# Performance work log

Hardware: AMD Instinct MI355X
Metric: run time of the kernel (lower is better)

## Reference

```python
import jax, jax.numpy as jnp
import numpy as np


def swish(x):
    return x * jax.nn.sigmoid(x)


def setup_inputs() -> dict:
    key = jax.random.key(0)
    ks = jax.random.split(key, 12)
    b, n, c, h, dg, hid = 4, 512, 256, 8, 6, 16

    def lin(k, i, o):
        return jax.random.normal(k, (i, o), jnp.float32) / np.float32(np.sqrt(i))

    return {
        "pairwise_g": jax.random.normal(ks[0], (b, n, n, dg), jnp.float32),
        "coset_functions": jax.random.normal(ks[1], (b, n, c), jnp.float32),
        "fc_q_w": lin(ks[2], c, c), "fc_q_b": jnp.zeros((c,), jnp.float32),
        "fc_k_w": lin(ks[3], c, c), "fc_k_b": jnp.zeros((c,), jnp.float32),
        "in_w": lin(ks[4], c, c), "in_b": jnp.zeros((c,), jnp.float32),
        "out_w": lin(ks[5], c, c), "out_b": jnp.zeros((c,), jnp.float32),
        "loc_w1": jax.random.normal(ks[6], (h, dg, hid), jnp.float32) / np.float32(np.sqrt(dg)),
        "loc_b1": jnp.zeros((h, hid), jnp.float32),
        "loc_w2": jax.random.normal(ks[7], (h, hid, hid), jnp.float32) / np.float32(np.sqrt(hid)),
        "loc_b2": jnp.zeros((h, hid), jnp.float32),
        "loc_w3": jax.random.normal(ks[8], (h, hid, 1), jnp.float32) / np.float32(np.sqrt(hid)),
        "loc_b3": jnp.zeros((h, 1), jnp.float32),
        "mask": jax.random.randint(ks[9], (4, 512), 0, 2) > 0,
    }


def reference(pairwise_g, coset_functions, fc_q_w, fc_q_b, fc_k_w, fc_k_b,
              in_w, in_b, out_w, out_b,
              loc_w1, loc_b1, loc_w2, loc_b2, loc_w3, loc_b3, mask):
    # nbhd_idx = arange(n) in the original (dense neighborhoods), so all
    # advanced-index gathers are identities and are expressed as broadcasts.
    b, n, c = coset_functions.shape
    h = loc_w1.shape[0]
    d = c // h

    # DotProductKernel: scores scaled by sqrt(embed_dim) = sqrt(c)
    Q = (coset_functions @ fc_q_w + fc_q_b).reshape(b, n, h, d)
    K = (coset_functions @ fc_k_w + fc_k_b).reshape(b, n, h, d)
    A_feat = jnp.einsum('bnhd,bmhd->bnmh', Q, K) / np.float32(np.sqrt(c))  # (b,n,m,h)

    # MultiheadWeightNet location kernel: per-head 3-layer MLP with swish
    # after every linear (LieConv-style LinearBNact blocks), out_dim=1.
    x = swish(jnp.einsum('bnmg,hgk->bnmhk', pairwise_g, loc_w1) + loc_b1)
    x = swish(jnp.einsum('bnmhk,hkj->bnmhj', x, loc_w2) + loc_b2)
    A_loc = swish(jnp.einsum('bnmhk,hko->bnmho', x, loc_w3) + loc_b3)[..., 0]  # (b,n,m,h)

    pre = A_loc + A_feat
    nbhd_mask = mask[:, None, :, None]          # mask over keys j: (b,1,m,1)
    pre = jnp.where(nbhd_mask, pre, jnp.float32(-1e38))
    att = jax.nn.softmax(pre, axis=2)           # softmax over neighbor dim m

    V = (coset_functions @ in_w + in_b).reshape(b, n, h, d)  # input_linear
    out = jnp.einsum('bnmh,bmhd->bnhd', att, V).reshape(b, n, c)
    return out @ out_w + out_b                  # output_linear; (b,n,c_out)
```

## Files before the change

### kernel.cpp

```cpp
#include <hip/hip_runtime.h>
#include <math.h>

namespace {

constexpr int kB = 4, kN = 512, kC = 256, kH = 8, kDG = 6, kHID = 16;

constexpr int S_QH = 20;
constexpr int S_W1 = 68;
constexpr int S_W2 = 132;
constexpr int S_B  = 17;
constexpr int S_AT = 516;

typedef _Float16 half2v __attribute__((ext_vector_type(2)));

__device__ __forceinline__ float swishf(float x) {
    return x * __builtin_amdgcn_rcpf(1.0f + __expf(-x));
}

__device__ __forceinline__ unsigned pk16(float a, float b) {
    unsigned short ha = __builtin_bit_cast(unsigned short, (_Float16)a);
    unsigned short hb = __builtin_bit_cast(unsigned short, (_Float16)b);
    return (unsigned)ha | ((unsigned)hb << 16);
}

__device__ __forceinline__ unsigned pkrtz(float a, float b) {
#if __has_builtin(__builtin_amdgcn_cvt_pkrtz)
    return __builtin_bit_cast(unsigned, __builtin_amdgcn_cvt_pkrtz(a, b));
#else
    return pk16(a, b);
#endif
}

__device__ __forceinline__ float fdot2u(unsigned a, unsigned b, float c) {
#if __has_builtin(__builtin_amdgcn_fdot2)
    return __builtin_amdgcn_fdot2(__builtin_bit_cast(half2v, a),
                                  __builtin_bit_cast(half2v, b), c, false);
#else
    half2v ha = __builtin_bit_cast(half2v, a);
    half2v hb = __builtin_bit_cast(half2v, b);
    return c + (float)ha[0] * (float)hb[0] + (float)ha[1] * (float)hb[1];
#endif
}

__global__ __launch_bounds__(256) void k_qkvc(
    const float* __restrict__ x,
    const float* __restrict__ wq, const float* __restrict__ bq,
    const float* __restrict__ wk, const float* __restrict__ bk,
    const float* __restrict__ wv, const float* __restrict__ bv,
    unsigned* __restrict__ Qh, unsigned* __restrict__ Kh,
    float* __restrict__ V,
    const unsigned char* __restrict__ mraw,
    int* __restrict__ list, int* __restrict__ meta) {
    const int t = threadIdx.x;

    if (blockIdx.x == 512) {
        __shared__ int s_isbool;
        if (t == 0) s_isbool = 0;
        __syncthreads();
        int found = 0;
        for (int i = t; i < kB * kN; i += 256)
            if ((i & 3) && mraw[i]) found = 1;
        if (found) atomicOr(&s_isbool, 1);
        __syncthreads();
        const int isb = s_isbool;
        const int b = t >> 6, lane = t & 63;
        const int* mi = (const int*)mraw;
        int base = 0;
        for (int c = 0; c < 8; ++c) {
            const int m = c * 64 + lane;
            const int idx = b * kN + m;
            const int valid = isb ? (mraw[idx] != 0) : (mi[idx] != 0);
            unsigned long long bal = __ballot(valid);
            int rank = (int)__popcll(bal & ((1ull << lane) - 1ull));
            if (valid) list[b * kN + base + rank] = m;
            base += (int)__popcll(bal);
        }
        for (int i = base + lane; i < kN; i += 64)
            list[b * kN + i] = (base == 0) ? i : 0;
        if (lane == 0) {
            meta[b] = (base == 0) ? kN : base;
            meta[4 + b] = (base == 0);
        }
        return;
    }

    __shared__ float sx[4][kC];
    const int r0 = blockIdx.x * 4;
    #pragma unroll
    for (int r = 0; r < 4; ++r) sx[r][t] = x[(r0 + r) * kC + t];
    __syncthreads();
    float aq[4] = {}, ak[4] = {}, av[4] = {};
    for (int k = 0; k < kC; ++k) {
        const float q = wq[k * kC + t];
        const float kk = wk[k * kC + t];
        const float v = wv[k * kC + t];
        #pragma unroll
        for (int r = 0; r < 4; ++r) {
            aq[r] += sx[r][k] * q;
            ak[r] += sx[r][k] * kk;
            av[r] += sx[r][k] * v;
        }
    }
    const float qb = bq[t], kb = bk[t], vb = bv[t];
    #pragma unroll
    for (int r = 0; r < 4; ++r) {
        const float qv = aq[r] + qb;
        const float kv = ak[r] + kb;
        V[(r0 + r) * kC + t] = av[r] + vb;
        const float qn = __shfl_down(qv, 1);
        const float kn = __shfl_down(kv, 1);
        if ((t & 1) == 0) {
            Qh[(r0 + r) * (kC / 2) + (t >> 1)] = pk16(qv, qn);
            Kh[(r0 + r) * (kC / 2) + (t >> 1)] = pk16(kv, kn);
        }
    }
}

__global__ __launch_bounds__(256, 4) void k_attn(
    const float* __restrict__ G,
    const unsigned* __restrict__ Qh,
    const unsigned* __restrict__ Kh,
    const float* __restrict__ V,
    const float* __restrict__ w1, const float* __restrict__ b1,
    const float* __restrict__ w2, const float* __restrict__ b2,
    const float* __restrict__ w3, const float* __restrict__ b3,
    const int* __restrict__ list, const int* __restrict__ meta,
    float* __restrict__ out) {
    __shared__ __align__(16) unsigned sQh[kH * S_QH];
    __shared__ __align__(16) uint4 sG4[kN];
    __shared__ int sList[kN];
    __shared__ __align__(16) unsigned sW1[kH * S_W1];
    __shared__ __align__(16) unsigned sW2[kH * S_W2];
    __shared__ float sB1[kH * S_B];
    __shared__ float sB2[kH * S_B];
    __shared__ float sW3[kH * S_B];
    __shared__ float sB3[kH];
    __shared__ float sAtt[kH * S_AT];
    __shared__ float sInv[kH];

    const int bn = blockIdx.x;
    const int b = bn >> 9;
    const int t = threadIdx.x;

    if (t < kH * S_QH) {
        const int h = t / S_QH, r = t % S_QH;
        sQh[t] = (r < 16) ? Qh[bn * (kC / 2) + h * 16 + r] : 0u;
    }
    sList[t] = list[b * kN + t];
    sList[t + 256] = list[b * kN + t + 256];
    #pragma unroll 1
    for (int rep = 0; rep < 2; ++rep) {
        const int m = t + rep * 256;
        const float* gp = G + ((size_t)bn * kN + m) * kDG;
        uint4 gw;
        gw.x = pkrtz(gp[0], gp[1]);
        gw.y = pkrtz(gp[2], gp[3]);
        gw.z = pkrtz(gp[4], gp[5]);
        gw.w = 0;
        sG4[m] = gw;
    }
    if (t < 128) {
        const int h = t >> 4, k = t & 15;
        const float* wp = w1 + (h * kDG) * kHID + k;
        sW1[h * S_W1 + k * 4 + 0] = pk16(wp[0], wp[16]);
        sW1[h * S_W1 + k * 4 + 1] = pk16(wp[32], wp[48]);
        sW1[h * S_W1 + k * 4 + 2] = pk16(wp[64], wp[80]);
        sW1[h * S_W1 + k * 4 + 3] = 0;
        sB1[h * S_B + k] = b1[h * kHID + k];
        sB2[h * S_B + k] = b2[h * kHID + k];
        sW3[h * S_B + k] = w3[h * kHID + k];
    } else {
        const int t2 = t - 128;
        const int h = t2 >> 4, j = t2 & 15;
        const float* wp = w2 + h * kHID * kHID + j;
        #pragma unroll
        for (int kp = 0; kp < 8; ++kp)
            sW2[h * S_W2 + j * 8 + kp] = pk16(wp[(2 * kp) * kHID], wp[(2 * kp + 1) * kHID]);
        if (j == 0) sB3[h] = b3[h];
    }
    const int nv = meta[b];
    const int allm = meta[4 + b];
    __syncthreads();

    const int items = nv * kH;
    #pragma unroll 1
    for (int base = 0; base < items; base += 256) {
        const int idx = base + t;
        if (idx < items) {
            const int h = idx & 7;
            const int mc = idx >> 3;
            const int m = sList[mc];
            const uint4 gw = sG4[m];
            const unsigned* khrow = Kh + ((size_t)(b * kN) + m) * (kC / 2) + h * 16;
            float af = 0.f;
            #pragma unroll
            for (int i = 0; i < 4; ++i) {
                const uint4 kv = ((const uint4*)khrow)[i];
                const uint4 qv = *(const uint4*)&sQh[h * S_QH + 4 * i];
                af = fdot2u(kv.x, qv.x, af);
                af = fdot2u(kv.y, qv.y, af);
                af = fdot2u(kv.z, qv.z, af);
                af = fdot2u(kv.w, qv.w, af);
            }
            unsigned xp[8];
            #pragma unroll
            for (int k2 = 0; k2 < 8; ++k2) {
                const uint4 wa = *(const uint4*)&sW1[h * S_W1 + (2 * k2) * 4];
                const uint4 wb = *(const uint4*)&sW1[h * S_W1 + (2 * k2 + 1) * 4];
                float aa = sB1[h * S_B + 2 * k2], ab = sB1[h * S_B + 2 * k2 + 1];
                aa = fdot2u(gw.x, wa.x, aa);
                aa = fdot2u(gw.y, wa.y, aa);
                aa = fdot2u(gw.z, wa.z, aa);
                ab = fdot2u(gw.x, wb.x, ab);
                ab = fdot2u(gw.y, wb.y, ab);
                ab = fdot2u(gw.z, wb.z, ab);
                xp[k2] = pkrtz(swishf(aa), swishf(ab));
            }
            float a3 = sB3[h];
            #pragma unroll
            for (int j = 0; j < kHID; ++j) {
                const uint4 w0 = *(const uint4*)&sW2[h * S_W2 + j * 8];
                const uint4 w1q = *(const uint4*)&sW2[h * S_W2 + j * 8 + 4];
                float acc = sB2[h * S_B + j];
                acc = fdot2u(xp[0], w0.x, acc);
                acc = fdot2u(xp[1], w0.y, acc);
                acc = fdot2u(xp[2], w0.z, acc);
                acc = fdot2u(xp[3], w0.w, acc);
                acc = fdot2u(xp[4], w1q.x, acc);
                acc = fdot2u(xp[5], w1q.y, acc);
                acc = fdot2u(xp[6], w1q.z, acc);
                acc = fdot2u(xp[7], w1q.w, acc);
                a3 += swishf(acc) * sW3[h * S_B + j];
            }
            sAtt[h * S_AT + mc] = allm ? 0.f : (swishf(a3) + af * 0.0625f);
        }
    }
    __syncthreads();

    {
        const int hg = t >> 5;
        const int lane = t & 31;
        const int nv4 = (nv + 3) & ~3;
        float mx = -3.4e38f;
        for (int idx = lane; idx < nv; idx += 32)
            mx = fmaxf(mx, sAtt[hg * S_AT + idx]);
        #pragma unroll
        for (int off = 16; off; off >>= 1)
            mx = fmaxf(mx, __shfl_xor(mx, off));
        float ls = 0.f;
        for (int idx = lane; idx < nv4; idx += 32) {
            const float e = (idx < nv) ? __expf(sAtt[hg * S_AT + idx] - mx) : 0.f;
            sAtt[hg * S_AT + idx] = e;
            ls += e;
        }
        #pragma unroll
        for (int off = 16; off; off >>= 1)
            ls += __shfl_xor(ls, off);
        if (lane == 0) sInv[hg] = 1.0f / ls;
    }
    __syncthreads();

    {
        const int h = t >> 5;
        const int dd = t & 31;
        const int nv4 = (nv + 3) & ~3;
        const float* vb = V + (size_t)b * kN * kC + h * 32 + dd;
        float a0 = 0.f, a1 = 0.f, a2 = 0.f, a3 = 0.f;
        for (int mc = 0; mc < nv4; mc += 4) {
            a0 += sAtt[h * S_AT + mc + 0] * vb[(size_t)sList[mc + 0] * kC];
            a1 += sAtt[h * S_AT + mc + 1] * vb[(size_t)sList[mc + 1] * kC];
            a2 += sAtt[h * S_AT + mc + 2] * vb[(size_t)sList[mc + 2] * kC];
            a3 += sAtt[h * S_AT + mc + 3] * vb[(size_t)sList[mc + 3] * kC];
        }
        out[bn * kC + t] = ((a0 + a1) + (a2 + a3)) * sInv[h];
    }
}

__global__ __launch_bounds__(256) void k_proj(
    const float* __restrict__ x,
    const float* __restrict__ w, const float* __restrict__ bias,
    float* __restrict__ y) {
    __shared__ float sx[8][kC];
    const int r0 = blockIdx.x * 8;
    const int t = threadIdx.x;
    #pragma unroll
    for (int r = 0; r < 8; ++r) sx[r][t] = x[(r0 + r) * kC + t];
    __syncthreads();
    float acc[8] = {};
    for (int k = 0; k < kC; ++k) {
        const float wv = w[k * kC + t];
        #pragma unroll
        for (int r = 0; r < 8; ++r) acc[r] += sx[r][k] * wv;
    }
    const float bb = bias[t];
    #pragma unroll
    for (int r = 0; r < 8; ++r) y[(r0 + r) * kC + t] = acc[r] + bb;
}

}

extern "C" void kernel_launch(void* const* d_in, const int* in_sizes, int n_in,
                              void* d_out, int out_size, void* d_ws, size_t ws_size,
                              hipStream_t stream) {
    (void)in_sizes; (void)n_in; (void)out_size; (void)ws_size;
    const float* G  = (const float*)d_in[0];
    const float* cf = (const float*)d_in[1];
    const float* wq = (const float*)d_in[2];
    const float* bq = (const float*)d_in[3];
    const float* wk = (const float*)d_in[4];
    const float* bk = (const float*)d_in[5];
    const float* wv = (const float*)d_in[6];
    const float* bv = (const float*)d_in[7];
    const float* wo = (const float*)d_in[8];
    const float* bo = (const float*)d_in[9];
    const float* w1 = (const float*)d_in[10];
    const float* b1 = (const float*)d_in[11];
    const float* w2 = (const float*)d_in[12];
    const float* b2 = (const float*)d_in[13];
    const float* w3 = (const float*)d_in[14];
    const float* b3 = (const float*)d_in[15];
    const unsigned char* mraw = (const unsigned char*)d_in[16];

    const int rows = kB * kN;
    unsigned* Qh = (unsigned*)d_ws;
    unsigned* Kh = Qh + (size_t)rows * (kC / 2);
    float* V = (float*)(Kh + (size_t)rows * (kC / 2));
    float* O = V + (size_t)rows * kC;
    int* list = (int*)(O + (size_t)rows * kC);
    int* meta = list + rows;

    k_qkvc<<<513, 256, 0, stream>>>(cf, wq, bq, wk, bk, wv, bv,
                                    Qh, Kh, V, mraw, list, meta);
    k_attn<<<rows, 256, 0, stream>>>(G, Qh, Kh, V, w1, b1, w2, b2, w3, b3,
                                     list, meta, O);
    k_proj<<<rows / 8, 256, 0, stream>>>(O, wo, bo, (float*)d_out);
}
```

Measured before the change: 248.8 us.

## Process two neighbors per thread with fixed head and load G only for valid keys

The attention kernel now fixes each thread's head and computes two masked-valid neighbors per iteration. This reuses weight and Q loads across both items and adds instruction-level parallelism. The G tile is no longer staged into shared memory for all 512 keys; only the rows for valid neighbors are read from global memory, which cuts memory traffic roughly in half with the random mask. The launch-bound occupancy hint rises to 5 blocks, and the QKV projection kernel does 8 rows per block instead of 4. The costs are higher register pressure and uncoalesced per-thread reads of G.

```diff
diff --git a/kernel.cpp b/kernel.cpp
--- a/kernel.cpp
+++ b/kernel.cpp
@@ -53,7 +53,7 @@
     int* __restrict__ list, int* __restrict__ meta) {
     const int t = threadIdx.x;
 
-    if (blockIdx.x == 512) {
+    if (blockIdx.x == 256) {
         __shared__ int s_isbool;
         if (t == 0) s_isbool = 0;
         __syncthreads();
@@ -84,18 +84,18 @@
         return;
     }
 
-    __shared__ float sx[4][kC];
-    const int r0 = blockIdx.x * 4;
+    __shared__ float sx[8][kC];
+    const int r0 = blockIdx.x * 8;
     #pragma unroll
-    for (int r = 0; r < 4; ++r) sx[r][t] = x[(r0 + r) * kC + t];
-    __syncthreads();
-    float aq[4] = {}, ak[4] = {}, av[4] = {};
+    for (int r = 0; r < 8; ++r) sx[r][t] = x[(r0 + r) * kC + t];
+    __syncthreads();
+    float aq[8] = {}, ak[8] = {}, av[8] = {};
     for (int k = 0; k < kC; ++k) {
         const float q = wq[k * kC + t];
         const float kk = wk[k * kC + t];
         const float v = wv[k * kC + t];
         #pragma unroll
-        for (int r = 0; r < 4; ++r) {
+        for (int r = 0; r < 8; ++r) {
             aq[r] += sx[r][k] * q;
             ak[r] += sx[r][k] * kk;
             av[r] += sx[r][k] * v;
@@ -103,7 +103,7 @@
     }
     const float qb = bq[t], kb = bk[t], vb = bv[t];
     #pragma unroll
-    for (int r = 0; r < 4; ++r) {
+    for (int r = 0; r < 8; ++r) {
         const float qv = aq[r] + qb;
         const float kv = ak[r] + kb;
         V[(r0 + r) * kC + t] = av[r] + vb;
@@ -116,7 +116,7 @@
     }
 }
 
-__global__ __launch_bounds__(256, 4) void k_attn(
+__global__ __launch_bounds__(256, 5) void k_attn(
     const float* __restrict__ G,
     const unsigned* __restrict__ Qh,
     const unsigned* __restrict__ Kh,
@@ -127,7 +127,6 @@
     const int* __restrict__ list, const int* __restrict__ meta,
     float* __restrict__ out) {
     __shared__ __align__(16) unsigned sQh[kH * S_QH];
-    __shared__ __align__(16) uint4 sG4[kN];
     __shared__ int sList[kN];
     __shared__ __align__(16) unsigned sW1[kH * S_W1];
     __shared__ __align__(16) unsigned sW2[kH * S_W2];
@@ -143,97 +142,130 @@
     const int t = threadIdx.x;
 
     if (t < kH * S_QH) {
-        const int h = t / S_QH, r = t % S_QH;
-        sQh[t] = (r < 16) ? Qh[bn * (kC / 2) + h * 16 + r] : 0u;
+        const int hh = t / S_QH, r = t % S_QH;
+        sQh[t] = (r < 16) ? Qh[bn * (kC / 2) + hh * 16 + r] : 0u;
     }
     sList[t] = list[b * kN + t];
     sList[t + 256] = list[b * kN + t + 256];
-    #pragma unroll 1
-    for (int rep = 0; rep < 2; ++rep) {
-        const int m = t + rep * 256;
-        const float* gp = G + ((size_t)bn * kN + m) * kDG;
-        uint4 gw;
-        gw.x = pkrtz(gp[0], gp[1]);
-        gw.y = pkrtz(gp[2], gp[3]);
-        gw.z = pkrtz(gp[4], gp[5]);
-        gw.w = 0;
-        sG4[m] = gw;
-    }
     if (t < 128) {
-        const int h = t >> 4, k = t & 15;
-        const float* wp = w1 + (h * kDG) * kHID + k;
-        sW1[h * S_W1 + k * 4 + 0] = pk16(wp[0], wp[16]);
-        sW1[h * S_W1 + k * 4 + 1] = pk16(wp[32], wp[48]);
-        sW1[h * S_W1 + k * 4 + 2] = pk16(wp[64], wp[80]);
-        sW1[h * S_W1 + k * 4 + 3] = 0;
-        sB1[h * S_B + k] = b1[h * kHID + k];
-        sB2[h * S_B + k] = b2[h * kHID + k];
-        sW3[h * S_B + k] = w3[h * kHID + k];
+        const int hh = t >> 4, k = t & 15;
+        const float* wp = w1 + (hh * kDG) * kHID + k;
+        sW1[hh * S_W1 + k * 4 + 0] = pk16(wp[0], wp[16]);
+        sW1[hh * S_W1 + k * 4 + 1] = pk16(wp[32], wp[48]);
+        sW1[hh * S_W1 + k * 4 + 2] = pk16(wp[64], wp[80]);
+        sW1[hh * S_W1 + k * 4 + 3] = 0;
+        sB1[hh * S_B + k] = b1[hh * kHID + k];
+        sB2[hh * S_B + k] = b2[hh * kHID + k];
+        sW3[hh * S_B + k] = w3[hh * kHID + k];
     } else {
         const int t2 = t - 128;
-        const int h = t2 >> 4, j = t2 & 15;
-        const float* wp = w2 + h * kHID * kHID + j;
+        const int hh = t2 >> 4, j = t2 & 15;
+        const float* wp = w2 + hh * kHID * kHID + j;
         #pragma unroll
         for (int kp = 0; kp < 8; ++kp)
-            sW2[h * S_W2 + j * 8 + kp] = pk16(wp[(2 * kp) * kHID], wp[(2 * kp + 1) * kHID]);
-        if (j == 0) sB3[h] = b3[h];
+            sW2[hh * S_W2 + j * 8 + kp] = pk16(wp[(2 * kp) * kHID], wp[(2 * kp + 1) * kHID]);
+        if (j == 0) sB3[hh] = b3[hh];
     }
     const int nv = meta[b];
     const int allm = meta[4 + b];
     __syncthreads();
 
-    const int items = nv * kH;
+    const int h = t & 7;
+    const int pr = t >> 3;
+    const unsigned* w1b = &sW1[h * S_W1];
+    const unsigned* w2b = &sW2[h * S_W2];
+    const float* b1b = &sB1[h * S_B];
+    const float* b2b = &sB2[h * S_B];
+    const float* w3b = &sW3[h * S_B];
+    const float b3r = sB3[h];
+    const uint4* qhb = (const uint4*)&sQh[h * S_QH];
+    const unsigned* khbase = Kh + (size_t)(b * kN) * (kC / 2) + h * 16;
+    const float* gbase = G + (size_t)bn * kN * kDG;
+    float* attb = &sAtt[h * S_AT];
+
     #pragma unroll 1
-    for (int base = 0; base < items; base += 256) {
-        const int idx = base + t;
-        if (idx < items) {
-            const int h = idx & 7;
-            const int mc = idx >> 3;
-            const int m = sList[mc];
-            const uint4 gw = sG4[m];
-            const unsigned* khrow = Kh + ((size_t)(b * kN) + m) * (kC / 2) + h * 16;
-            float af = 0.f;
-            #pragma unroll
-            for (int i = 0; i < 4; ++i) {
-                const uint4 kv = ((const uint4*)khrow)[i];
-                const uint4 qv = *(const uint4*)&sQh[h * S_QH + 4 * i];
-                af = fdot2u(kv.x, qv.x, af);
-                af = fdot2u(kv.y, qv.y, af);
-                af = fdot2u(kv.z, qv.z, af);
-                af = fdot2u(kv.w, qv.w, af);
-            }
-            unsigned xp[8];
-            #pragma unroll
-            for (int k2 = 0; k2 < 8; ++k2) {
-                const uint4 wa = *(const uint4*)&sW1[h * S_W1 + (2 * k2) * 4];
-                const uint4 wb = *(const uint4*)&sW1[h * S_W1 + (2 * k2 + 1) * 4];
-                float aa = sB1[h * S_B + 2 * k2], ab = sB1[h * S_B + 2 * k2 + 1];
-                aa = fdot2u(gw.x, wa.x, aa);
-                aa = fdot2u(gw.y, wa.y, aa);
-                aa = fdot2u(gw.z, wa.z, aa);
-                ab = fdot2u(gw.x, wb.x, ab);
-                ab = fdot2u(gw.y, wb.y, ab);
-                ab = fdot2u(gw.z, wb.z, ab);
-                xp[k2] = pkrtz(swishf(aa), swishf(ab));
-            }
-            float a3 = sB3[h];
-            #pragma unroll
-            for (int j = 0; j < kHID; ++j) {
-                const uint4 w0 = *(const uint4*)&sW2[h * S_W2 + j * 8];
-                const uint4 w1q = *(const uint4*)&sW2[h * S_W2 + j * 8 + 4];
-                float acc = sB2[h * S_B + j];
-                acc = fdot2u(xp[0], w0.x, acc);
-                acc = fdot2u(xp[1], w0.y, acc);
-                acc = fdot2u(xp[2], w0.z, acc);
-                acc = fdot2u(xp[3], w0.w, acc);
-                acc = fdot2u(xp[4], w1q.x, acc);
-                acc = fdot2u(xp[5], w1q.y, acc);
-                acc = fdot2u(xp[6], w1q.z, acc);
-                acc = fdot2u(xp[7], w1q.w, acc);
-                a3 += swishf(acc) * sW3[h * S_B + j];
-            }
-            sAtt[h * S_AT + mc] = allm ? 0.f : (swishf(a3) + af * 0.0625f);
-        }
+    for (int p0 = 0; p0 < nv; p0 += 64) {
+        const int pA = p0 + pr, pB = pA + 32;
+        const int cA = min(pA, nv - 1), cB = min(pB, nv - 1);
+        const int mA = sList[cA], mB = sList[cB];
+        const float* gpA = gbase + (size_t)mA * kDG;
+        const float* gpB = gbase + (size_t)mB * kDG;
+        const uint4* khA = (const uint4*)(khbase + (size_t)mA * (kC / 2));
+        const uint4* khB = (const uint4*)(khbase + (size_t)mB * (kC / 2));
+        float afA = 0.f, afB = 0.f;
+        #pragma unroll
+        for (int i = 0; i < 4; ++i) {
+            const uint4 qv = qhb[i];
+            const uint4 ka = khA[i];
+            const uint4 kb2 = khB[i];
+            afA = fdot2u(ka.x, qv.x, afA);
+            afA = fdot2u(ka.y, qv.y, afA);
+            afA = fdot2u(ka.z, qv.z, afA);
+            afA = fdot2u(ka.w, qv.w, afA);
+            afB = fdot2u(kb2.x, qv.x, afB);
+            afB = fdot2u(kb2.y, qv.y, afB);
+            afB = fdot2u(kb2.z, qv.z, afB);
+            afB = fdot2u(kb2.w, qv.w, afB);
+        }
+        const unsigned gAx = pkrtz(gpA[0], gpA[1]);
+        const unsigned gAy = pkrtz(gpA[2], gpA[3]);
+        const unsigned gAz = pkrtz(gpA[4], gpA[5]);
+        const unsigned gBx = pkrtz(gpB[0], gpB[1]);
+        const unsigned gBy = pkrtz(gpB[2], gpB[3]);
+        const unsigned gBz = pkrtz(gpB[4], gpB[5]);
+        unsigned xpA[8], xpB[8];
+        #pragma unroll
+        for (int k2 = 0; k2 < 8; ++k2) {
+            const uint4 wa = *(const uint4*)&w1b[8 * k2];
+            const uint4 wb = *(const uint4*)&w1b[8 * k2 + 4];
+            const float ba = b1b[2 * k2], bb = b1b[2 * k2 + 1];
+            float aaA = ba, abA = bb, aaB = ba, abB = bb;
+            aaA = fdot2u(gAx, wa.x, aaA);
+            aaA = fdot2u(gAy, wa.y, aaA);
+            aaA = fdot2u(gAz, wa.z, aaA);
+            abA = fdot2u(gAx, wb.x, abA);
+            abA = fdot2u(gAy, wb.y, abA);
+            abA = fdot2u(gAz, wb.z, abA);
+            aaB = fdot2u(gBx, wa.x, aaB);
+            aaB = fdot2u(gBy, wa.y, aaB);
+            aaB = fdot2u(gBz, wa.z, aaB);
+            abB = fdot2u(gBx, wb.x, abB);
+            abB = fdot2u(gBy, wb.y, abB);
+            abB = fdot2u(gBz, wb.z, abB);
+            xpA[k2] = pkrtz(swishf(aaA), swishf(abA));
+            xpB[k2] = pkrtz(swishf(aaB), swishf(abB));
+        }
+        float a3A = b3r, a3B = b3r;
+        #pragma unroll
+        for (int j = 0; j < kHID; ++j) {
+            const uint4 w0 = *(const uint4*)&w2b[j * 8];
+            const uint4 w1q = *(const uint4*)&w2b[j * 8 + 4];
+            const float bj = b2b[j];
+            float accA = bj, accB = bj;
+            accA = fdot2u(xpA[0], w0.x, accA);
+            accA = fdot2u(xpA[1], w0.y, accA);
+            accA = fdot2u(xpA[2], w0.z, accA);
+            accA = fdot2u(xpA[3], w0.w, accA);
+            accA = fdot2u(xpA[4], w1q.x, accA);
+            accA = fdot2u(xpA[5], w1q.y, accA);
+            accA = fdot2u(xpA[6], w1q.z, accA);
+            accA = fdot2u(xpA[7], w1q.w, accA);
+            accB = fdot2u(xpB[0], w0.x, accB);
+            accB = fdot2u(xpB[1], w0.y, accB);
+            accB = fdot2u(xpB[2], w0.z, accB);
+            accB = fdot2u(xpB[3], w0.w, accB);
+            accB = fdot2u(xpB[4], w1q.x, accB);
+            accB = fdot2u(xpB[5], w1q.y, accB);
+            accB = fdot2u(xpB[6], w1q.z, accB);
+            accB = fdot2u(xpB[7], w1q.w, accB);
+            const float wj = w3b[j];
+            a3A += swishf(accA) * wj;
+            a3B += swishf(accB) * wj;
+        }
+        const float valA = swishf(a3A) + afA * 0.0625f;
+        const float valB = swishf(a3B) + afB * 0.0625f;
+        if (pA < nv) attb[cA] = allm ? 0.f : valA;
+        if (pB < nv) attb[cB] = allm ? 0.f : valB;
     }
     __syncthreads();
 
@@ -261,18 +293,18 @@
     __syncthreads();
 
     {
-        const int h = t >> 5;
+        const int hg = t >> 5;
         const int dd = t & 31;
         const int nv4 = (nv + 3) & ~3;
-        const float* vb = V + (size_t)b * kN * kC + h * 32 + dd;
+        const float* vb = V + (size_t)b * kN * kC + hg * 32 + dd;
         float a0 = 0.f, a1 = 0.f, a2 = 0.f, a3 = 0.f;
         for (int mc = 0; mc < nv4; mc += 4) {
-            a0 += sAtt[h * S_AT + mc + 0] * vb[(size_t)sList[mc + 0] * kC];
-            a1 += sAtt[h * S_AT + mc + 1] * vb[(size_t)sList[mc + 1] * kC];
-            a2 += sAtt[h * S_AT + mc + 2] * vb[(size_t)sList[mc + 2] * kC];
-            a3 += sAtt[h * S_AT + mc + 3] * vb[(size_t)sList[mc + 3] * kC];
-        }
-        out[bn * kC + t] = ((a0 + a1) + (a2 + a3)) * sInv[h];
+            a0 += sAtt[hg * S_AT + mc + 0] * vb[(size_t)sList[mc + 0] * kC];
+            a1 += sAtt[hg * S_AT + mc + 1] * vb[(size_t)sList[mc + 1] * kC];
+            a2 += sAtt[hg * S_AT + mc + 2] * vb[(size_t)sList[mc + 2] * kC];
+            a3 += sAtt[hg * S_AT + mc + 3] * vb[(size_t)sList[mc + 3] * kC];
+        }
+        out[bn * kC + t] = ((a0 + a1) + (a2 + a3)) * sInv[hg];
     }
 }
 
@@ -329,7 +361,7 @@
     int* list = (int*)(O + (size_t)rows * kC);
     int* meta = list + rows;
 
-    k_qkvc<<<513, 256, 0, stream>>>(cf, wq, bq, wk, bk, wv, bv,
+    k_qkvc<<<257, 256, 0, stream>>>(cf, wq, bq, wk, bk, wv, bv,
                                     Qh, Kh, V, mraw, list, meta);
     k_attn<<<rows, 256, 0, stream>>>(G, Qh, Kh, V, w1, b1, w2, b2, w3, b3,
                                      list, meta, O);
```

New measurement: 829.4 us. 233% more time.

## Run location MLP and QK scores on MFMA, store V in fp16

Applied to the files above, without the earlier changes.

Replaces the per-thread fdot2 evaluation of the per-head 3-layer location MLP and Q·K dot products with 16x16x16 f16 MFMA instructions. Each wave processes 16 neighbours per tile, with first- and second-layer weights held in registers as MFMA A fragments. V is now written as packed fp16 and the attention-weighted sum reads half2 values, halving V traffic. The QKV projection kernel processes 8 rows per block, halving its block count. Risks include extra register pressure from keeping 16 half4 fragments per thread, wasted MFMA lanes on the padded K dimension, and reduced precision in V.

```diff
diff --git a/kernel.cpp b/kernel.cpp
--- a/kernel.cpp
+++ b/kernel.cpp
@@ -6,12 +6,13 @@
 constexpr int kB = 4, kN = 512, kC = 256, kH = 8, kDG = 6, kHID = 16;
 
 constexpr int S_QH = 20;
-constexpr int S_W1 = 68;
-constexpr int S_W2 = 132;
-constexpr int S_B  = 17;
+constexpr int S_BT = 20;
 constexpr int S_AT = 516;
 
 typedef _Float16 half2v __attribute__((ext_vector_type(2)));
+typedef _Float16 half4v __attribute__((ext_vector_type(4)));
+typedef float float4v __attribute__((ext_vector_type(4)));
+typedef unsigned uint2v __attribute__((ext_vector_type(2)));
 
 __device__ __forceinline__ float swishf(float x) {
     return x * __builtin_amdgcn_rcpf(1.0f + __expf(-x));
@@ -24,22 +25,11 @@
 }
 
 __device__ __forceinline__ unsigned pkrtz(float a, float b) {
-#if __has_builtin(__builtin_amdgcn_cvt_pkrtz)
     return __builtin_bit_cast(unsigned, __builtin_amdgcn_cvt_pkrtz(a, b));
-#else
-    return pk16(a, b);
-#endif
-}
-
-__device__ __forceinline__ float fdot2u(unsigned a, unsigned b, float c) {
-#if __has_builtin(__builtin_amdgcn_fdot2)
-    return __builtin_amdgcn_fdot2(__builtin_bit_cast(half2v, a),
-                                  __builtin_bit_cast(half2v, b), c, false);
-#else
-    half2v ha = __builtin_bit_cast(half2v, a);
-    half2v hb = __builtin_bit_cast(half2v, b);
-    return c + (float)ha[0] * (float)hb[0] + (float)ha[1] * (float)hb[1];
-#endif
+}
+
+__device__ __forceinline__ float4v mfma16(half4v a, half4v b, float4v c) {
+    return __builtin_amdgcn_mfma_f32_16x16x16f16(a, b, c, 0, 0, 0);
 }
 
 __global__ __launch_bounds__(256) void k_qkvc(
@@ -48,12 +38,12 @@
     const float* __restrict__ wk, const float* __restrict__ bk,
     const float* __restrict__ wv, const float* __restrict__ bv,
     unsigned* __restrict__ Qh, unsigned* __restrict__ Kh,
-    float* __restrict__ V,
+    unsigned* __restrict__ Vh,
     const unsigned char* __restrict__ mraw,
     int* __restrict__ list, int* __restrict__ meta) {
     const int t = threadIdx.x;
 
-    if (blockIdx.x == 512) {
+    if (blockIdx.x == 256) {
         __shared__ int s_isbool;
         if (t == 0) s_isbool = 0;
         __syncthreads();
@@ -84,18 +74,18 @@
         return;
     }
 
-    __shared__ float sx[4][kC];
-    const int r0 = blockIdx.x * 4;
-    #pragma unroll
-    for (int r = 0; r < 4; ++r) sx[r][t] = x[(r0 + r) * kC + t];
-    __syncthreads();
-    float aq[4] = {}, ak[4] = {}, av[4] = {};
+    __shared__ float sx[8][kC];
+    const int r0 = blockIdx.x * 8;
+    #pragma unroll
+    for (int r = 0; r < 8; ++r) sx[r][t] = x[(r0 + r) * kC + t];
+    __syncthreads();
+    float aq[8] = {}, ak[8] = {}, av[8] = {};
     for (int k = 0; k < kC; ++k) {
         const float q = wq[k * kC + t];
         const float kk = wk[k * kC + t];
         const float v = wv[k * kC + t];
         #pragma unroll
-        for (int r = 0; r < 4; ++r) {
+        for (int r = 0; r < 8; ++r) {
             aq[r] += sx[r][k] * q;
             ak[r] += sx[r][k] * kk;
             av[r] += sx[r][k] * v;
@@ -103,15 +93,17 @@
     }
     const float qb = bq[t], kb = bk[t], vb = bv[t];
     #pragma unroll
-    for (int r = 0; r < 4; ++r) {
+    for (int r = 0; r < 8; ++r) {
         const float qv = aq[r] + qb;
         const float kv = ak[r] + kb;
-        V[(r0 + r) * kC + t] = av[r] + vb;
+        const float vv = av[r] + vb;
         const float qn = __shfl_down(qv, 1);
         const float kn = __shfl_down(kv, 1);
+        const float vn = __shfl_down(vv, 1);
         if ((t & 1) == 0) {
             Qh[(r0 + r) * (kC / 2) + (t >> 1)] = pk16(qv, qn);
             Kh[(r0 + r) * (kC / 2) + (t >> 1)] = pk16(kv, kn);
+            Vh[(r0 + r) * (kC / 2) + (t >> 1)] = pk16(vv, vn);
         }
     }
 }
@@ -120,7 +112,7 @@
     const float* __restrict__ G,
     const unsigned* __restrict__ Qh,
     const unsigned* __restrict__ Kh,
-    const float* __restrict__ V,
+    const unsigned* __restrict__ Vh,
     const float* __restrict__ w1, const float* __restrict__ b1,
     const float* __restrict__ w2, const float* __restrict__ b2,
     const float* __restrict__ w3, const float* __restrict__ b3,
@@ -129,11 +121,9 @@
     __shared__ __align__(16) unsigned sQh[kH * S_QH];
     __shared__ __align__(16) uint4 sG4[kN];
     __shared__ int sList[kN];
-    __shared__ __align__(16) unsigned sW1[kH * S_W1];
-    __shared__ __align__(16) unsigned sW2[kH * S_W2];
-    __shared__ float sB1[kH * S_B];
-    __shared__ float sB2[kH * S_B];
-    __shared__ float sW3[kH * S_B];
+    __shared__ __align__(16) float sB1T[kH * S_BT];
+    __shared__ __align__(16) float sB2T[kH * S_BT];
+    __shared__ __align__(16) float sW3T[kH * S_BT];
     __shared__ float sB3[kH];
     __shared__ float sAtt[kH * S_AT];
     __shared__ float sInv[kH];
@@ -141,10 +131,26 @@
     const int bn = blockIdx.x;
     const int b = bn >> 9;
     const int t = threadIdx.x;
+    const int l = t & 63;
+    const int p = l & 15;
+    const int s = l >> 4;
+    const int wid = t >> 6;
+
+    half4v a1f[kH], a2f[kH];
+    #pragma unroll
+    for (int h = 0; h < kH; ++h) {
+        #pragma unroll
+        for (int r = 0; r < 4; ++r) {
+            const int k = 4 * s + r;
+            a1f[h][r] = (k < kDG) ? (_Float16)w1[(h * kDG + k) * kHID + p]
+                                  : (_Float16)0.f;
+            a2f[h][r] = (_Float16)w2[(h * kHID + k) * kHID + p];
+        }
+    }
 
     if (t < kH * S_QH) {
-        const int h = t / S_QH, r = t % S_QH;
-        sQh[t] = (r < 16) ? Qh[bn * (kC / 2) + h * 16 + r] : 0u;
+        const int hh = t / S_QH, r = t % S_QH;
+        sQh[t] = (r < 16) ? Qh[bn * (kC / 2) + hh * 16 + r] : 0u;
     }
     sList[t] = list[b * kN + t];
     sList[t + 256] = list[b * kN + t + 256];
@@ -160,79 +166,59 @@
         sG4[m] = gw;
     }
     if (t < 128) {
-        const int h = t >> 4, k = t & 15;
-        const float* wp = w1 + (h * kDG) * kHID + k;
-        sW1[h * S_W1 + k * 4 + 0] = pk16(wp[0], wp[16]);
-        sW1[h * S_W1 + k * 4 + 1] = pk16(wp[32], wp[48]);
-        sW1[h * S_W1 + k * 4 + 2] = pk16(wp[64], wp[80]);
-        sW1[h * S_W1 + k * 4 + 3] = 0;
-        sB1[h * S_B + k] = b1[h * kHID + k];
-        sB2[h * S_B + k] = b2[h * kHID + k];
-        sW3[h * S_B + k] = w3[h * kHID + k];
-    } else {
-        const int t2 = t - 128;
-        const int h = t2 >> 4, j = t2 & 15;
-        const float* wp = w2 + h * kHID * kHID + j;
-        #pragma unroll
-        for (int kp = 0; kp < 8; ++kp)
-            sW2[h * S_W2 + j * 8 + kp] = pk16(wp[(2 * kp) * kHID], wp[(2 * kp + 1) * kHID]);
-        if (j == 0) sB3[h] = b3[h];
+        const int hh = t >> 4, j = t & 15;
+        sB1T[hh * S_BT + j] = b1[hh * kHID + j];
+        sB2T[hh * S_BT + j] = b2[hh * kHID + j];
+        sW3T[hh * S_BT + j] = w3[hh * kHID + j];
+        if (j == 0) sB3[hh] = b3[hh];
     }
     const int nv = meta[b];
     const int allm = meta[4 + b];
     __syncthreads();
 
-    const int items = nv * kH;
-    #pragma unroll 1
-    for (int base = 0; base < items; base += 256) {
-        const int idx = base + t;
-        if (idx < items) {
-            const int h = idx & 7;
-            const int mc = idx >> 3;
+    const unsigned* khB = Kh + (size_t)(b * kN) * (kC / 2);
+    const int ntiles = (nv + 15) >> 4;
+
+    #pragma unroll
+    for (int h = 0; h < kH; ++h) {
+        const float4v bv1 = *(const float4v*)&sB1T[h * S_BT + s * 4];
+        const float4v bv2 = *(const float4v*)&sB2T[h * S_BT + s * 4];
+        const float4v w3f = *(const float4v*)&sW3T[h * S_BT + s * 4];
+        half4v w3h;
+        #pragma unroll
+        for (int r = 0; r < 4; ++r) w3h[r] = (_Float16)w3f[r];
+        const float b3s = sB3[h];
+        const float4v b3v = {b3s, b3s, b3s, b3s};
+        const uint2v q0u = {sQh[h * S_QH + 2 * s], sQh[h * S_QH + 2 * s + 1]};
+        const uint2v q1u = {sQh[h * S_QH + 8 + 2 * s], sQh[h * S_QH + 9 + 2 * s]};
+        const half4v qA0 = __builtin_bit_cast(half4v, q0u);
+        const half4v qA1 = __builtin_bit_cast(half4v, q1u);
+
+        #pragma unroll 1
+        for (int tile = wid; tile < ntiles; tile += 4) {
+            const int mcw = tile * 16 + p;
+            const int mc = min(mcw, nv - 1);
             const int m = sList[mc];
-            const uint4 gw = sG4[m];
-            const unsigned* khrow = Kh + ((size_t)(b * kN) + m) * (kC / 2) + h * 16;
-            float af = 0.f;
-            #pragma unroll
-            for (int i = 0; i < 4; ++i) {
-                const uint4 kv = ((const uint4*)khrow)[i];
-                const uint4 qv = *(const uint4*)&sQh[h * S_QH + 4 * i];
-                af = fdot2u(kv.x, qv.x, af);
-                af = fdot2u(kv.y, qv.y, af);
-                af = fdot2u(kv.z, qv.z, af);
-                af = fdot2u(kv.w, qv.w, af);
-            }
-            unsigned xp[8];
-            #pragma unroll
-            for (int k2 = 0; k2 < 8; ++k2) {
-                const uint4 wa = *(const uint4*)&sW1[h * S_W1 + (2 * k2) * 4];
-                const uint4 wb = *(const uint4*)&sW1[h * S_W1 + (2 * k2 + 1) * 4];
-                float aa = sB1[h * S_B + 2 * k2], ab = sB1[h * S_B + 2 * k2 + 1];
-                aa = fdot2u(gw.x, wa.x, aa);
-                aa = fdot2u(gw.y, wa.y, aa);
-                aa = fdot2u(gw.z, wa.z, aa);
-                ab = fdot2u(gw.x, wb.x, ab);
-                ab = fdot2u(gw.y, wb.y, ab);
-                ab = fdot2u(gw.z, wb.z, ab);
-                xp[k2] = pkrtz(swishf(aa), swishf(ab));
-            }
-            float a3 = sB3[h];
-            #pragma unroll
-            for (int j = 0; j < kHID; ++j) {
-                const uint4 w0 = *(const uint4*)&sW2[h * S_W2 + j * 8];
-                const uint4 w1q = *(const uint4*)&sW2[h * S_W2 + j * 8 + 4];
-                float acc = sB2[h * S_B + j];
-                acc = fdot2u(xp[0], w0.x, acc);
-                acc = fdot2u(xp[1], w0.y, acc);
-                acc = fdot2u(xp[2], w0.z, acc);
-                acc = fdot2u(xp[3], w0.w, acc);
-                acc = fdot2u(xp[4], w1q.x, acc);
-                acc = fdot2u(xp[5], w1q.y, acc);
-                acc = fdot2u(xp[6], w1q.z, acc);
-                acc = fdot2u(xp[7], w1q.w, acc);
-                a3 += swishf(acc) * sW3[h * S_B + j];
-            }
-            sAtt[h * S_AT + mc] = allm ? 0.f : (swishf(a3) + af * 0.0625f);
+            const unsigned* gp = (const unsigned*)&sG4[m];
+            uint2v gu = {gp[(s & 1) * 2], gp[(s & 1) * 2 + 1]};
+            if (s >= 2) { gu[0] = 0u; gu[1] = 0u; }
+            const half4v bg = __builtin_bit_cast(half4v, gu);
+            const float4v c1 = mfma16(a1f[h], bg, bv1);
+            const uint2v x1u = {pkrtz(swishf(c1[0]), swishf(c1[1])),
+                                pkrtz(swishf(c1[2]), swishf(c1[3]))};
+            const float4v c2 = mfma16(a2f[h], __builtin_bit_cast(half4v, x1u), bv2);
+            const uint2v x2u = {pkrtz(swishf(c2[0]), swishf(c2[1])),
+                                pkrtz(swishf(c2[2]), swishf(c2[3]))};
+            const float4v c3 = mfma16(w3h, __builtin_bit_cast(half4v, x2u), b3v);
+            const unsigned* kr = khB + (size_t)m * (kC / 2) + h * 16 + 2 * s;
+            const uint2v k0 = {kr[0], kr[1]};
+            const uint2v k1 = {kr[8], kr[9]};
+            float4v ca = {0.f, 0.f, 0.f, 0.f};
+            ca = mfma16(qA0, __builtin_bit_cast(half4v, k0), ca);
+            ca = mfma16(qA1, __builtin_bit_cast(half4v, k1), ca);
+            const float pre = swishf(c3[0]) + ca[0] * 0.0625f;
+            if (s == 0 && mcw < nv)
+                sAtt[h * S_AT + mcw] = allm ? 0.f : pre;
         }
     }
     __syncthreads();
@@ -240,7 +226,6 @@
     {
         const int hg = t >> 5;
         const int lane = t & 31;
-        const int nv4 = (nv + 3) & ~3;
         float mx = -3.4e38f;
         for (int idx = lane; idx < nv; idx += 32)
             mx = fmaxf(mx, sAtt[hg * S_AT + idx]);
@@ -248,8 +233,8 @@
         for (int off = 16; off; off >>= 1)
             mx = fmaxf(mx, __shfl_xor(mx, off));
         float ls = 0.f;
-        for (int idx = lane; idx < nv4; idx += 32) {
-            const float e = (idx < nv) ? __expf(sAtt[hg * S_AT + idx] - mx) : 0.f;
+        for (int idx = lane; idx < nv; idx += 32) {
+            const float e = __expf(sAtt[hg * S_AT + idx] - mx);
             sAtt[hg * S_AT + idx] = e;
             ls += e;
         }
@@ -261,18 +246,32 @@
     __syncthreads();
 
     {
-        const int h = t >> 5;
-        const int dd = t & 31;
-        const int nv4 = (nv + 3) & ~3;
-        const float* vb = V + (size_t)b * kN * kC + h * 32 + dd;
-        float a0 = 0.f, a1 = 0.f, a2 = 0.f, a3 = 0.f;
-        for (int mc = 0; mc < nv4; mc += 4) {
-            a0 += sAtt[h * S_AT + mc + 0] * vb[(size_t)sList[mc + 0] * kC];
-            a1 += sAtt[h * S_AT + mc + 1] * vb[(size_t)sList[mc + 1] * kC];
-            a2 += sAtt[h * S_AT + mc + 2] * vb[(size_t)sList[mc + 2] * kC];
-            a3 += sAtt[h * S_AT + mc + 3] * vb[(size_t)sList[mc + 3] * kC];
-        }
-        out[bn * kC + t] = ((a0 + a1) + (a2 + a3)) * sInv[h];
+        const int hg = t >> 5;
+        const int dp = (t >> 1) & 15;
+        const int par = t & 1;
+        const unsigned* vbp = Vh + (size_t)(b * kN) * (kC / 2) + hg * 16 + dp;
+        float alo = 0.f, ahi = 0.f, blo = 0.f, bhi = 0.f;
+        int mc = par;
+        for (; mc + 2 < nv; mc += 4) {
+            const float aw0 = sAtt[hg * S_AT + mc];
+            const float aw1 = sAtt[hg * S_AT + mc + 2];
+            const half2v v0 = __builtin_bit_cast(half2v, vbp[(size_t)sList[mc] * (kC / 2)]);
+            const half2v v1 = __builtin_bit_cast(half2v, vbp[(size_t)sList[mc + 2] * (kC / 2)]);
+            alo += aw0 * (float)v0[0];
+            ahi += aw0 * (float)v0[1];
+            blo += aw1 * (float)v1[0];
+            bhi += aw1 * (float)v1[1];
+        }
+        for (; mc < nv; mc += 2) {
+            const float aw = sAtt[hg * S_AT + mc];
+            const half2v vv = __builtin_bit_cast(half2v, vbp[(size_t)sList[mc] * (kC / 2)]);
+            alo += aw * (float)vv[0];
+            ahi += aw * (float)vv[1];
+        }
+        alo += blo; ahi += bhi;
+        alo += __shfl_xor(alo, 1);
+        ahi += __shfl_xor(ahi, 1);
+        out[bn * kC + t] = (par ? ahi : alo) * sInv[hg];
     }
 }
 
@@ -324,14 +323,14 @@
     const int rows = kB * kN;
     unsigned* Qh = (unsigned*)d_ws;
     unsigned* Kh = Qh + (size_t)rows * (kC / 2);
-    float* V = (float*)(Kh + (size_t)rows * (kC / 2));
-    float* O = V + (size_t)rows * kC;
+    unsigned* Vh = Kh + (size_t)rows * (kC / 2);
+    float* O = (float*)(Vh + (size_t)rows * (kC / 2));
     int* list = (int*)(O + (size_t)rows * kC);
     int* meta = list + rows;
 
-    k_qkvc<<<513, 256, 0, stream>>>(cf, wq, bq, wk, bk, wv, bv,
-                                    Qh, Kh, V, mraw, list, meta);
-    k_attn<<<rows, 256, 0, stream>>>(G, Qh, Kh, V, w1, b1, w2, b2, w3, b3,
+    k_qkvc<<<257, 256, 0, stream>>>(cf, wq, bq, wk, bk, wv, bv,
+                                    Qh, Kh, Vh, mraw, list, meta);
+    k_attn<<<rows, 256, 0, stream>>>(G, Qh, Kh, Vh, w1, b1, w2, b2, w3, b3,
                                      list, meta, O);
     k_proj<<<rows / 8, 256, 0, stream>>>(O, wo, bo, (float*)d_out);
 }
```

Measured after the change: 264.1 us. 1.06x slower.
